# Performance work log

Hardware: AMD Instinct MI355X
Metric: run time of the kernel (lower is better)

Reference implementation:

```python
import jax, jax.numpy as jnp
import numpy as np

N_HEADS = 8


def _norm_weights(idx):
    # softmax over where(idx>0, 1, -9e15) along axis 1 -> uniform weights over non-pad slots
    logits = jnp.where(idx > 0, jnp.float32(1.0), jnp.float32(-9e15))
    return jax.nn.softmax(logits, axis=1)


def _layer_norm(x, g, b, eps=1e-6):
    mu = jnp.mean(x, axis=-1, keepdims=True)
    var = jnp.var(x, axis=-1, keepdims=True)
    return (x - mu) * jax.lax.rsqrt(var + eps) * g + b


def _mha_block(x, mask, wq, wk, wv, wo, g, b):
    # standard multi-head self-attention block with residual + layernorm
    B, L, D = x.shape
    hd = D // N_HEADS
    q = (x @ wq).reshape(B, L, N_HEADS, hd)
    k = (x @ wk).reshape(B, L, N_HEADS, hd)
    v = (x @ wv).reshape(B, L, N_HEADS, hd)
    scores = jnp.einsum('bqhd,bkhd->bhqk', q, k) / jnp.float32(np.sqrt(hd))
    scores = jnp.where(mask[:, None, None, :], jnp.float32(-1e9), scores)
    attn = jax.nn.softmax(scores, axis=-1)
    out = jnp.einsum('bhqk,bkhd->bqhd', attn, v).reshape(B, L, D) @ wo
    return _layer_norm(out + x, g, b)


def _forward(data_idx, seq, timestamps, user_level, useq, user_inf, user_cen,
             spread_status, id2vector,
             user_emb, cen_emb, time_emb, pos_emb, inf_emb,
             w1, w2, w3,
             t_wq, t_wk, t_wv, t_wo, t_g, t_b,
             s_wq, s_wk, s_wv, s_wo, s_g, s_b,
             W, W2, f_l1_w, f_l1_b, f_l2_w, f_l2_b, lin_w, lin_b):
    # ---- HGNN layer (hypergraph conv) ----
    tv = w3[0]  # TextVector = weight3[0]
    dot = w3 @ tv
    cos = dot / (jnp.linalg.norm(tv) * jnp.linalg.norm(w3, axis=1))
    inter_nw = jnp.mean(cos)  # scalar

    tweet_hidden = user_emb + cen_emb[user_cen]          # [N, D]
    x = (tweet_hidden @ w1) * inter_nw                   # [N, D]
    nor = _norm_weights(seq)                             # [E, L]
    edge = jnp.einsum('elc,el->ec', x[seq], nor)         # gather + weighted reduce
    edge = jax.nn.relu(edge)
    e1 = edge @ w2                                       # [E, D]
    u_nor = _norm_weights(useq)                          # [N, Lu]
    node = jnp.einsum('nlc,nl->nc', e1[useq], u_nor)     # [N, D]

    # ---- HGSL head ----
    sb = seq[data_idx]                                   # [B, L]
    nor_b = _norm_weights(sb)
    att_mask = sb == 0                                   # PAD == 0
    adj = node[sb]                                       # [B, L, D]

    att_hidden = adj + time_emb[timestamps[data_idx]]
    att_out = _mha_block(att_hidden, att_mask, t_wq, t_wk, t_wv, t_wo, t_g, t_b)
    news = jnp.einsum('blc,bl->bc', att_out, nor_b)
    news = jnp.concatenate([news, spread_status[data_idx][:, 2:] / 3600.0 / 24.0], axis=-1) @ W

    att_hidden_s = adj + inf_emb[user_inf[data_idx]] + pos_emb[user_level[data_idx]]
    att_out_s = _mha_block(att_hidden_s, att_mask, s_wq, s_wk, s_wv, s_wo, s_g, s_b)
    news_s = jnp.einsum('blc,bl->bc', att_out_s, nor_b)
    news_s = jnp.concatenate([news_s, spread_status[data_idx][:, :2]], axis=-1) @ W2

    # Gated fusion (linear3 unused in original forward; id2vector is overwritten/unused)
    emb = jnp.stack([news, news_s], axis=0)              # [2, B, D+2]
    score = jax.nn.softmax(jnp.tanh(emb @ f_l1_w + f_l1_b) @ f_l2_w + f_l2_b, axis=0)
    fused = jnp.sum(score * emb, axis=0)                 # [B, D+2]
    return jax.nn.log_softmax(fused @ lin_w + lin_b, axis=1)


def setup_inputs():
    key = jax.random.key(0)
    ks = jax.random.split(key, 40)
    N, E, L, Lu, D, B, TV = 50000, 10000, 50, 20, 128, 512, 768
    Dw = D + 2
    s = 0.05
    inp = {
        'data_idx': jax.random.randint(ks[0], (B,), 0, E),
        'seq': jax.random.randint(ks[1], (E, L), 0, N),
        'timestamps': jax.random.randint(ks[2], (E, L), 0, 5000),
        'user_level': jax.random.randint(ks[3], (E, L), 0, 50),
        'useq': jax.random.randint(ks[4], (N, Lu), 0, E),
        'user_inf': jax.random.randint(ks[5], (E, L), 0, 200),
        'user_cen': jax.random.randint(ks[6], (N,), 0, 600),
        'spread_status': jax.random.uniform(ks[7], (E, 4), dtype=jnp.float32),
        'id2vector': jax.random.normal(ks[8], (1,), dtype=jnp.float32),
        'user_emb': s * jax.random.normal(ks[9], (N, D), dtype=jnp.float32),
        'cen_emb': s * jax.random.normal(ks[10], (600, D), dtype=jnp.float32),
        'time_emb': s * jax.random.normal(ks[11], (5000, D), dtype=jnp.float32),
        'pos_emb': s * jax.random.normal(ks[12], (50, D), dtype=jnp.float32),
        'inf_emb': s * jax.random.normal(ks[13], (200, D), dtype=jnp.float32),
        'w1': s * jax.random.normal(ks[14], (D, D), dtype=jnp.float32),
        'w2': s * jax.random.normal(ks[15], (D, D), dtype=jnp.float32),
        'w3': s * jax.random.normal(ks[16], (TV, TV), dtype=jnp.float32),
        'W': s * jax.random.normal(ks[17], (Dw, Dw), dtype=jnp.float32),
        'W2': s * jax.random.normal(ks[18], (Dw, Dw), dtype=jnp.float32),
        'f_l1_w': s * jax.random.normal(ks[19], (Dw, Dw), dtype=jnp.float32),
        'f_l1_b': jnp.zeros((Dw,), jnp.float32),
        'f_l2_w': s * jax.random.normal(ks[20], (Dw, 1), dtype=jnp.float32),
        'f_l2_b': jnp.zeros((1,), jnp.float32),
        'lin_w': s * jax.random.normal(ks[21], (Dw, 2), dtype=jnp.float32),
        'lin_b': jnp.zeros((2,), jnp.float32),
    }
    for nm, i in [('t', 22), ('s', 27)]:
        inp[nm + '_wq'] = s * jax.random.normal(ks[i], (D, D), dtype=jnp.float32)
        inp[nm + '_wk'] = s * jax.random.normal(ks[i + 1], (D, D), dtype=jnp.float32)
        inp[nm + '_wv'] = s * jax.random.normal(ks[i + 2], (D, D), dtype=jnp.float32)
        inp[nm + '_wo'] = s * jax.random.normal(ks[i + 3], (D, D), dtype=jnp.float32)
        inp[nm + '_g'] = jnp.ones((D,), jnp.float32)
        inp[nm + '_b'] = jnp.zeros((D,), jnp.float32)
    return inp


def reference(data_idx, seq, timestamps, user_level, useq, user_inf, user_cen,
              spread_status, id2vector,
              user_emb, cen_emb, time_emb, pos_emb, inf_emb,
              w1, w2, w3,
              t_wq, t_wk, t_wv, t_wo, t_g, t_b,
              s_wq, s_wk, s_wv, s_wo, s_g, s_b,
              W, W2, f_l1_w, f_l1_b, f_l2_w, f_l2_b, lin_w, lin_b):
    return _forward(data_idx, seq, timestamps, user_level, useq, user_inf, user_cen,
                    spread_status, id2vector,
                    user_emb, cen_emb, time_emb, pos_emb, inf_emb,
                    w1, w2, w3,
                    t_wq, t_wk, t_wv, t_wo, t_g, t_b,
                    s_wq, s_wk, s_wv, s_wo, s_g, s_b,
                    W, W2, f_l1_w, f_l1_b, f_l2_w, f_l2_b, lin_w, lin_b)
```

## Files before the change

kernel.cpp:

```cpp
#include <hip/hip_runtime.h>
#include <math.h>

constexpr int Nn = 50000;
constexpr int Ee = 10000;
constexpr int Ll = 50;
constexpr int LuU = 20;
constexpr int Dd = 128;
constexpr int Bb = 512;
constexpr int TVv = 768;
constexpr int Dw = 130;
constexpr int BL = Bb * Ll;
constexpr int BLP = Bb * 64;

typedef __attribute__((ext_vector_type(8))) short bf8v;
typedef __attribute__((ext_vector_type(4))) float f4v;
typedef __attribute__((ext_vector_type(8))) unsigned short u16x8;
typedef __attribute__((ext_vector_type(4))) unsigned short u16x4;

__device__ __forceinline__ unsigned short f2bf(float f) {
  union { float f; unsigned u; } v; v.f = f;
  unsigned r = v.u + 0x7FFFu + ((v.u >> 16) & 1u);
  return (unsigned short)(r >> 16);
}
__device__ __forceinline__ float bf2f(unsigned short h) {
  union { unsigned u; float f; } v; v.u = ((unsigned)h) << 16; return v.f;
}
__device__ __forceinline__ int swz(int b) { return b ^ (((b >> 8) & 7) << 4); }
__device__ __forceinline__ int swz7(int b) { return b ^ (((b >> 7) & 7) << 4); }

__device__ __forceinline__ float block_sum_256(float v, volatile float* scr) {
#pragma unroll
  for (int o = 32; o > 0; o >>= 1) v += __shfl_down(v, o, 64);
  __syncthreads();
  if ((threadIdx.x & 63) == 0) scr[threadIdx.x >> 6] = v;
  __syncthreads();
  return scr[0] + scr[1] + scr[2] + scr[3];
}

__global__ __launch_bounds__(256) void k_cos(const float* __restrict__ w3,
                                             float* __restrict__ dotb,
                                             float* __restrict__ nrmb) {
  __shared__ float scr[4];
  int i = blockIdx.x;
  const float* row = w3 + (size_t)i * TVv;
  float d = 0.f, n = 0.f;
  for (int j = threadIdx.x; j < TVv; j += 256) {
    float a = row[j];
    d += a * w3[j];
    n += a * a;
  }
  d = block_sum_256(d, scr);
  n = block_sum_256(n, scr);
  if (threadIdx.x == 0) { dotb[i] = d; nrmb[i] = n; }
}

__global__ __launch_bounds__(256) void k_internw(const float* __restrict__ dotb,
                                                 const float* __restrict__ nrmb,
                                                 float* __restrict__ internw) {
  __shared__ float scr[4];
  float n0 = sqrtf(nrmb[0]);
  float s = 0.f;
  for (int i = threadIdx.x; i < TVv; i += 256)
    s += dotb[i] / (n0 * sqrtf(nrmb[i]));
  s = block_sum_256(s, scr);
  if (threadIdx.x == 0) *internw = s / (float)TVv;
}

__global__ __launch_bounds__(256) void k_prep(
    const float* w1, const float* w2,
    const float* twq, const float* twk, const float* twv, const float* two,
    const float* swq, const float* swk, const float* swv, const float* swo,
    unsigned short* __restrict__ out) {
  int wsel = blockIdx.x >> 3, part = blockIdx.x & 7;
  const float* w;
  switch (wsel) {
    case 0: w = w1; break;  case 1: w = w2; break;
    case 2: w = twq; break; case 3: w = twk; break;
    case 4: w = twv; break; case 5: w = two; break;
    case 6: w = swq; break; case 7: w = swk; break;
    case 8: w = swv; break; default: w = swo; break;
  }
  int u = part * 256 + threadIdx.x;
  int n = u >> 4, k0 = (u & 15) * 8;
  u16x8 pv;
#pragma unroll
  for (int i = 0; i < 8; i++) pv[i] = f2bf(w[(size_t)(k0 + i) * Dd + n]);
  ((u16x8*)(out + (size_t)wsel * Dd * Dd))[u] = pv;
}

__global__ __launch_bounds__(256) void k_th(const float* __restrict__ ue,
                                            const float* __restrict__ ce,
                                            const int* __restrict__ ucen,
                                            unsigned short* __restrict__ TH) {
  int r = blockIdx.x * 16 + (threadIdx.x >> 4);
  int c0 = (threadIdx.x & 15) * 8;
  int cen = ucen[r];
  const float4* up = (const float4*)(ue + (size_t)r * Dd + c0);
  const float4* cp = (const float4*)(ce + (size_t)cen * Dd + c0);
  float4 u0 = up[0], u1 = up[1], v0 = cp[0], v1 = cp[1];
  float a[8] = {u0.x + v0.x, u0.y + v0.y, u0.z + v0.z, u0.w + v0.w,
                u1.x + v1.x, u1.y + v1.y, u1.z + v1.z, u1.w + v1.w};
  u16x8 o;
#pragma unroll
  for (int i = 0; i < 8; i++) o[i] = f2bf(a[i]);
  *(u16x8*)(TH + (size_t)r * Dd + c0) = o;
}

template <int RELU>
__global__ __launch_bounds__(256) void k_gather(const unsigned short* __restrict__ X,
                                                const int* __restrict__ idx,
                                                unsigned short* __restrict__ out) {
  int r = blockIdx.x * 16 + (threadIdx.x >> 4);
  int c0 = (threadIdx.x & 15) * 8;
  const int* row = idx + (size_t)r * Ll;
  float acc[8];
#pragma unroll
  for (int i = 0; i < 8; i++) acc[i] = 0.f;
  int cnt = 0;
#pragma unroll 1
  for (int l0 = 0; l0 < Ll; l0 += 10) {
    int ids[10];
#pragma unroll
    for (int t = 0; t < 10; t++) ids[t] = row[l0 + t];
    u16x8 vv[10];
#pragma unroll
    for (int t = 0; t < 10; t++)
      vv[t] = *(const u16x8*)(X + (size_t)ids[t] * Dd + c0);
#pragma unroll
    for (int t = 0; t < 10; t++)
      if (ids[t] > 0) {
        cnt++;
#pragma unroll
        for (int i = 0; i < 8; i++) acc[i] += bf2f(vv[t][i]);
      }
  }
  u16x8 ov;
  if (cnt) {
    float inv = 1.f / (float)cnt;
#pragma unroll
    for (int i = 0; i < 8; i++) {
      float v = acc[i] * inv;
      if (RELU) v = fmaxf(v, 0.f);
      ov[i] = f2bf(v);
    }
  } else {
    u16x8 x0 = *(const u16x8*)(X + c0);
#pragma unroll
    for (int i = 0; i < 8; i++) {
      float v = bf2f(x0[i]);
      if (RELU) v = fmaxf(v, 0.f);
      ov[i] = f2bf(v);
    }
  }
  *(u16x8*)(out + (size_t)r * Dd + c0) = ov;
}

template <int EPI>
__global__ __launch_bounds__(256) void k_gemm_plain(
    const unsigned short* __restrict__ inA, const float* __restrict__ scalep,
    const unsigned short* __restrict__ WTg,
    unsigned short* __restrict__ out, int nrows) {
  __shared__ unsigned short WT[Dd * Dd];
  __shared__ __align__(16) unsigned short Ab[64 * Dd];
  int tid = threadIdx.x;
  float sc = (EPI == 1) ? *scalep : 1.f;
  {
    const u16x8* src = (const u16x8*)WTg;
    for (int u = tid; u < 2048; u += 256)
      *(u16x8*)((char*)WT + swz(u * 16)) = src[u];
  }
  int r0 = blockIdx.x * 64;
  for (int u = tid; u < 1024; u += 256) {
    int rr = u >> 4;
    int r = r0 + rr;
    u16x8 pv;
    if (r < nrows) pv = ((const u16x8*)inA)[(size_t)r * 16 + (u & 15)];
    else {
#pragma unroll
      for (int i = 0; i < 8; i++) pv[i] = 0;
    }
    *(u16x8*)((char*)Ab + swz(rr * 256 + (u & 15) * 16)) = pv;
  }
  __syncthreads();
  int lane = tid & 63, wid = tid >> 6;
  int lrow = lane & 15, lg = lane >> 4;
  bf8v af[4];
#pragma unroll
  for (int kc = 0; kc < 4; kc++)
    af[kc] = *(const bf8v*)((char*)Ab + swz((wid * 16 + lrow) * 256 + kc * 64 + lg * 16));
  f4v acc[8];
#pragma unroll
  for (int nt = 0; nt < 8; nt++)
#pragma unroll
    for (int j = 0; j < 4; j++) acc[nt][j] = 0.f;
#pragma unroll
  for (int nt = 0; nt < 8; nt++)
#pragma unroll
    for (int kc = 0; kc < 4; kc++) {
      bf8v bfg = *(const bf8v*)((char*)WT + swz((nt * 16 + lrow) * 256 + kc * 64 + lg * 16));
      acc[nt] = __builtin_amdgcn_mfma_f32_16x16x32_bf16(af[kc], bfg, acc[nt], 0, 0, 0);
    }
#pragma unroll
  for (int nt = 0; nt < 8; nt++)
#pragma unroll
    for (int j = 0; j < 4; j++) {
      int r = r0 + wid * 16 + lg * 4 + j;
      if (r < nrows) {
        float v = acc[nt][j];
        if (EPI == 1) v = fmaxf(v * sc, 0.f);
        out[(size_t)r * Dd + nt * 16 + lrow] = f2bf(v);
      }
    }
}

__global__ __launch_bounds__(256) void k_hidfuse(
    const unsigned short* __restrict__ E1, const int* __restrict__ data_idx,
    const int* __restrict__ seq, const int* __restrict__ tsmp,
    const int* __restrict__ uinf, const int* __restrict__ ulev,
    const int* __restrict__ useq,
    const float* __restrict__ time_emb, const float* __restrict__ inf_emb,
    const float* __restrict__ pos_emb,
    unsigned short* __restrict__ hidTb, unsigned short* __restrict__ hidSb) {
  int bl = blockIdx.x * 16 + (threadIdx.x >> 4);
  int c0 = (threadIdx.x & 15) * 8;
  int b = bl / Ll, l = bl % Ll;
  int e = data_idx[b];
  int sid = seq[(size_t)e * Ll + l];
  const int* urow = useq + (size_t)sid * LuU;
  float acc[8];
#pragma unroll
  for (int i = 0; i < 8; i++) acc[i] = 0.f;
  int cnt = 0;
#pragma unroll 1
  for (int t0 = 0; t0 < LuU; t0 += 10) {
    int ids[10];
#pragma unroll
    for (int t = 0; t < 10; t++) ids[t] = urow[t0 + t];
    u16x8 vv[10];
#pragma unroll
    for (int t = 0; t < 10; t++)
      vv[t] = *(const u16x8*)(E1 + (size_t)ids[t] * Dd + c0);
#pragma unroll
    for (int t = 0; t < 10; t++)
      if (ids[t] > 0) {
        cnt++;
#pragma unroll
        for (int i = 0; i < 8; i++) acc[i] += bf2f(vv[t][i]);
      }
  }
  float node[8];
  if (cnt) {
    float inv = 1.f / (float)cnt;
#pragma unroll
    for (int i = 0; i < 8; i++) node[i] = acc[i] * inv;
  } else {
    u16x8 e0 = *(const u16x8*)(E1 + c0);
#pragma unroll
    for (int i = 0; i < 8; i++) node[i] = bf2f(e0[i]);
  }
  int ts = tsmp[(size_t)e * Ll + l];
  int fi = uinf[(size_t)e * Ll + l];
  int lv = ulev[(size_t)e * Ll + l];
  const float4* tp = (const float4*)(time_emb + (size_t)ts * Dd + c0);
  const float4* ip = (const float4*)(inf_emb + (size_t)fi * Dd + c0);
  const float4* pp = (const float4*)(pos_emb + (size_t)lv * Dd + c0);
  float4 t0 = tp[0], t1 = tp[1];
  float4 i0 = ip[0], i1 = ip[1];
  float4 p0 = pp[0], p1 = pp[1];
  float te[8] = {t0.x, t0.y, t0.z, t0.w, t1.x, t1.y, t1.z, t1.w};
  float ie[8] = {i0.x, i0.y, i0.z, i0.w, i1.x, i1.y, i1.z, i1.w};
  float pe[8] = {p0.x, p0.y, p0.z, p0.w, p1.x, p1.y, p1.z, p1.w};
  u16x8 ht, hs;
#pragma unroll
  for (int i = 0; i < 8; i++) {
    ht[i] = f2bf(node[i] + te[i]);
    hs[i] = f2bf(node[i] + ie[i] + pe[i]);
  }
  size_t o = (size_t)bl * Dd + c0;
  *(u16x8*)(hidTb + o) = ht;
  *(u16x8*)(hidSb + o) = hs;
}

__global__ __launch_bounds__(256, 3) void k_qkvattn(
    const unsigned short* __restrict__ hidT, const unsigned short* __restrict__ hidS,
    const unsigned short* __restrict__ WTbase,
    const int* __restrict__ data_idx, const int* __restrict__ seq,
    unsigned short* __restrict__ ctxp) {
  __shared__ __align__(16) char LDS[49152];
  char* Qs  = LDS;
  char* Ks  = LDS + 16384;
  char* VTs = LDS + 32768;

  int b = blockIdx.x, branch = blockIdx.y;
  int tid = threadIdx.x, lane = tid & 63, wid = tid >> 6;
  int lrow = lane & 15, lg = lane >> 4;
  const unsigned short* hid = (branch ? hidS : hidT) + (size_t)b * Ll * Dd;
  const unsigned short* Wq = WTbase + (size_t)(2 + branch * 4) * Dd * Dd;
  const unsigned short* Wk = Wq + Dd * Dd;
  const unsigned short* Wv = Wk + Dd * Dd;

  int e = data_idx[b];
  int mi = (lane < Ll) ? (seq[(size_t)e * Ll + lane] == 0 ? 1 : 0) : 2;
  int mflag[4][4];
#pragma unroll
  for (int mt = 0; mt < 4; mt++)
#pragma unroll
    for (int j = 0; j < 4; j++)
      mflag[mt][j] = __shfl(mi, mt * 16 + lg * 4 + j, 64);

  bf8v hf[4][4];
#pragma unroll
  for (int qt = 0; qt < 4; qt++) {
    int q = qt * 16 + lrow;
#pragma unroll
    for (int kc = 0; kc < 4; kc++) {
      bf8v v;
      if (q < Ll) v = *(const bf8v*)(hid + (size_t)q * Dd + kc * 32 + lg * 8);
      else {
#pragma unroll
        for (int i = 0; i < 8; i++) v[i] = 0;
      }
      hf[qt][kc] = v;
    }
  }

#pragma unroll
  for (int sel = 0; sel < 2; sel++) {
    const unsigned short* W = sel ? Wk : Wq;
    char* Dst = sel ? Ks : Qs;
#pragma unroll
    for (int n2 = 0; n2 < 2; n2++) {
      int n = wid * 2 + n2;
      bf8v wf[4];
#pragma unroll
      for (int kc = 0; kc < 4; kc++)
        wf[kc] = *(const bf8v*)(W + (size_t)(n * 16 + lrow) * Dd + kc * 32 + lg * 8);
#pragma unroll
      for (int qt = 0; qt < 4; qt++) {
        f4v a = {0.f, 0.f, 0.f, 0.f};
#pragma unroll
        for (int kc = 0; kc < 4; kc++)
          a = __builtin_amdgcn_mfma_f32_16x16x32_bf16(wf[kc], hf[qt][kc], a, 0, 0, 0);
        u16x4 o;
#pragma unroll
        for (int j = 0; j < 4; j++) o[j] = f2bf(a[j]);
        *(u16x4*)(Dst + swz((qt * 16 + lrow) * 256 + n * 32 + lg * 8)) = o;
      }
    }
  }
  {
    bf8v hv[4];
    int kvq = wid * 16 + lrow;
#pragma unroll
    for (int kc = 0; kc < 4; kc++) {
      bf8v v;
      if (kvq < Ll) v = *(const bf8v*)(hid + (size_t)kvq * Dd + kc * 32 + lg * 8);
      else {
#pragma unroll
        for (int i = 0; i < 8; i++) v[i] = 0;
      }
      hv[kc] = v;
    }
#pragma unroll
    for (int nt = 0; nt < 8; nt++) {
      bf8v wf[4];
#pragma unroll
      for (int kc = 0; kc < 4; kc++)
        wf[kc] = *(const bf8v*)(Wv + (size_t)(nt * 16 + lrow) * Dd + kc * 32 + lg * 8);
      f4v a = {0.f, 0.f, 0.f, 0.f};
#pragma unroll
      for (int kc = 0; kc < 4; kc++)
        a = __builtin_amdgcn_mfma_f32_16x16x32_bf16(hv[kc], wf[kc], a, 0, 0, 0);
      u16x4 o;
#pragma unroll
      for (int j = 0; j < 4; j++) o[j] = f2bf(a[j]);
      *(u16x4*)(VTs + swz7((nt * 16 + lrow) * 128 + (wid * 16 + lg * 4) * 2)) = o;
    }
  }
  bf8v af[2][4], bq[2][4];
#pragma unroll
  for (int hi = 0; hi < 2; hi++) {
    int h = wid * 2 + hi;
#pragma unroll
    for (int t = 0; t < 4; t++) {
      bf8v a, q;
      if (lg < 2) {
        a = *(const bf8v*)(Ks + swz((t * 16 + lrow) * 256 + h * 32 + lg * 16));
        q = *(const bf8v*)(Qs + swz((t * 16 + lrow) * 256 + h * 32 + lg * 16));
      } else {
#pragma unroll
        for (int i = 0; i < 8; i++) { a[i] = 0; q[i] = 0; }
      }
      af[hi][t] = a; bq[hi][t] = q;
    }
  }
  __syncthreads();

  char* PTw = LDS + wid * 8192;
  size_t rbase = ((size_t)branch * Bb + b) * 64;
#pragma unroll
  for (int hi = 0; hi < 2; hi++) {
    int h = wid * 2 + hi;
#pragma unroll
    for (int nt = 0; nt < 4; nt++) {
      f4v sa[4];
#pragma unroll
      for (int mt = 0; mt < 4; mt++)
#pragma unroll
        for (int j = 0; j < 4; j++) sa[mt][j] = 0.f;
#pragma unroll
      for (int mt = 0; mt < 4; mt++)
        sa[mt] = __builtin_amdgcn_mfma_f32_16x16x32_bf16(af[hi][mt], bq[hi][nt], sa[mt], 0, 0, 0);
      float m = -3.0e38f;
#pragma unroll
      for (int mt = 0; mt < 4; mt++)
#pragma unroll
        for (int j = 0; j < 4; j++) {
          int mk = mflag[mt][j];
          float v = sa[mt][j] * 0.25f;
          v = (mk == 1) ? -1e9f : v;
          v = (mk == 2) ? -3.0e38f : v;
          sa[mt][j] = v;
          m = fmaxf(m, v);
        }
      m = fmaxf(m, __shfl_xor(m, 16, 64));
      m = fmaxf(m, __shfl_xor(m, 32, 64));
      float s = 0.f;
#pragma unroll
      for (int mt = 0; mt < 4; mt++)
#pragma unroll
        for (int j = 0; j < 4; j++) {
          float p = expf(sa[mt][j] - m);
          sa[mt][j] = p;
          s += p;
        }
      s += __shfl_xor(s, 16, 64);
      s += __shfl_xor(s, 32, 64);
      float inv = 1.f / s;
      int q = nt * 16 + lrow;
#pragma unroll
      for (int mt = 0; mt < 4; mt++) {
        u16x4 pw;
#pragma unroll
        for (int j = 0; j < 4; j++) pw[j] = f2bf(sa[mt][j] * inv);
        *(u16x4*)(PTw + swz7(q * 128 + mt * 32 + lg * 8)) = pw;
      }
    }
    f4v pacc[4];
#pragma unroll
    for (int nt = 0; nt < 4; nt++)
#pragma unroll
      for (int j = 0; j < 4; j++) pacc[nt][j] = 0.f;
#pragma unroll
    for (int kt = 0; kt < 2; kt++) {
      bf8v av = *(const bf8v*)(VTs + swz7((h * 16 + lrow) * 128 + kt * 64 + lg * 16));
#pragma unroll
      for (int nt = 0; nt < 4; nt++) {
        bf8v bv = *(const bf8v*)(PTw + swz7((nt * 16 + lrow) * 128 + kt * 64 + lg * 16));
        pacc[nt] = __builtin_amdgcn_mfma_f32_16x16x32_bf16(av, bv, pacc[nt], 0, 0, 0);
      }
    }
#pragma unroll
    for (int nt = 0; nt < 4; nt++) {
      int q = nt * 16 + lrow;
      unsigned* cp = (unsigned*)(ctxp + (rbase + q) * Dd + h * 16 + lg * 4);
      cp[0] = (unsigned)f2bf(pacc[nt][0]) | ((unsigned)f2bf(pacc[nt][1]) << 16);
      cp[1] = (unsigned)f2bf(pacc[nt][2]) | ((unsigned)f2bf(pacc[nt][3]) << 16);
    }
  }
}

__global__ __launch_bounds__(256) void k_gemm_lnnews(
    const unsigned short* __restrict__ ctxp,
    const unsigned short* __restrict__ hidT, const unsigned short* __restrict__ hidS,
    const unsigned short* __restrict__ WTbase,
    const float* __restrict__ tg, const float* __restrict__ tb,
    const float* __restrict__ sg, const float* __restrict__ sb_,
    const int* __restrict__ data_idx, const int* __restrict__ seq,
    const float* __restrict__ spread,
    float* __restrict__ news) {
  __shared__ unsigned short WT[Dd * Dd];
  __shared__ __align__(16) char UB[64 * 132 * 4];
  __shared__ int sl[Ll];
  __shared__ int scnt;
  unsigned short* Ab = (unsigned short*)UB;
  float (*O)[132] = (float (*)[132])UB;

  int b = blockIdx.x & 511, branch = blockIdx.x >> 9;
  const unsigned short* resid = (branch ? hidS : hidT);
  const unsigned short* Wg = WTbase + (size_t)(5 + branch * 4) * Dd * Dd;
  const float* lng = branch ? sg : tg;
  const float* lnb = branch ? sb_ : tb;
  int tid = threadIdx.x;
  int e = data_idx[b];
  if (tid < Ll) sl[tid] = seq[(size_t)e * Ll + tid];

  {
    const u16x8* src = (const u16x8*)Wg;
    for (int u = tid; u < 2048; u += 256)
      *(u16x8*)((char*)WT + swz(u * 16)) = src[u];
  }
  for (int u = tid; u < 1024; u += 256) {
    int rr = u >> 4;
    u16x8 pv = ((const u16x8*)ctxp)[(((size_t)branch * Bb + b) * 64 + rr) * 16 + (u & 15)];
    *(u16x8*)((char*)Ab + swz(rr * 256 + (u & 15) * 16)) = pv;
  }
  __syncthreads();

  int lane = tid & 63, wid = tid >> 6;
  int lrow = lane & 15, lg = lane >> 4;
  bf8v af[4];
#pragma unroll
  for (int kc = 0; kc < 4; kc++)
    af[kc] = *(const bf8v*)((char*)Ab + swz((wid * 16 + lrow) * 256 + kc * 64 + lg * 16));
  f4v acc[8];
#pragma unroll
  for (int nt = 0; nt < 8; nt++)
#pragma unroll
    for (int j = 0; j < 4; j++) acc[nt][j] = 0.f;
#pragma unroll
  for (int nt = 0; nt < 8; nt++)
#pragma unroll
    for (int kc = 0; kc < 4; kc++) {
      bf8v bfg = *(const bf8v*)((char*)WT + swz((nt * 16 + lrow) * 256 + kc * 64 + lg * 16));
      acc[nt] = __builtin_amdgcn_mfma_f32_16x16x32_bf16(af[kc], bfg, acc[nt], 0, 0, 0);
    }
  __syncthreads();
#pragma unroll
  for (int nt = 0; nt < 8; nt++)
#pragma unroll
    for (int j = 0; j < 4; j++)
      O[wid * 16 + lg * 4 + j][nt * 16 + lrow] = acc[nt][j];
  __syncthreads();
  int r = tid >> 2, c0 = (tid & 3) * 32;
  if (r < Ll) {
    size_t gr = (size_t)b * Ll + r;
    float vv[32];
    float s1 = 0.f, s2 = 0.f;
#pragma unroll
    for (int i8 = 0; i8 < 4; i8++) {
      u16x8 hb = *(const u16x8*)(resid + gr * Dd + c0 + i8 * 8);
#pragma unroll
      for (int i = 0; i < 8; i++) {
        float x = O[r][c0 + i8 * 8 + i] + bf2f(hb[i]);
        vv[i8 * 8 + i] = x; s1 += x; s2 += x * x;
      }
    }
    s1 += __shfl_xor(s1, 1, 64); s2 += __shfl_xor(s2, 1, 64);
    s1 += __shfl_xor(s1, 2, 64); s2 += __shfl_xor(s2, 2, 64);
    float mu = s1 * (1.f / Dd);
    float var = s2 * (1.f / Dd) - mu * mu;
    float rs = rsqrtf(var + 1e-6f);
#pragma unroll
    for (int i = 0; i < 32; i++) {
      int c = c0 + i;
      O[r][c] = (vv[i] - mu) * rs * lng[c] + lnb[c];
    }
  }
  if (tid == 0) {
    int c = 0;
    for (int l = 0; l < Ll; l++) c += (sl[l] > 0);
    scnt = c;
  }
  __syncthreads();
  float* nrow = news + ((size_t)branch * Bb + b) * 132;
  if (tid < Dd) {
    int cnt = scnt;
    float wnp = cnt ? 1.f / (float)cnt : 0.02f;
    float a = 0.f;
    for (int l = 0; l < Ll; l++) {
      float w = cnt ? ((sl[l] > 0) ? wnp : 0.f) : wnp;
      a += w * O[l][tid];
    }
    nrow[tid] = a;
  } else if (tid < Dw) {
    int cc = tid - Dd;
    nrow[tid] = branch ? spread[(size_t)e * 4 + cc]
                       : spread[(size_t)e * 4 + 2 + cc] * (1.f / 86400.f);
  }
}

__global__ __launch_bounds__(256) void k_newsW(const float* __restrict__ news,
                                               const float* __restrict__ Wm,
                                               const float* __restrict__ W2m,
                                               float* __restrict__ NT,
                                               float* __restrict__ NS) {
  __shared__ float Wl[Dw][Dw + 1];
  __shared__ float nrow[132];
  int branch = blockIdx.y;
  const float* W = branch ? W2m : Wm;
  float* out = branch ? NS : NT;
  for (int u = threadIdx.x; u < Dw * Dw; u += 256)
    Wl[u / Dw][u % Dw] = W[u];
  for (int rr = 0; rr < 32; rr++) {
    int b = blockIdx.x * 32 + rr;
    __syncthreads();
    if (threadIdx.x < Dw)
      nrow[threadIdx.x] = news[((size_t)branch * Bb + b) * 132 + threadIdx.x];
    __syncthreads();
    int j = threadIdx.x;
    if (j < Dw) {
      float acc = 0.f;
      for (int kk = 0; kk < Dw; kk++) acc += nrow[kk] * Wl[kk][j];
      out[(size_t)b * Dw + j] = acc;
    }
  }
}

__global__ __launch_bounds__(256) void k_fusion(const float* __restrict__ nt,
                                                const float* __restrict__ ns,
                                                const float* __restrict__ l1w,
                                                const float* __restrict__ l1b,
                                                const float* __restrict__ l2w,
                                                const float* __restrict__ l2b,
                                                const float* __restrict__ linw,
                                                const float* __restrict__ linb,
                                                float* __restrict__ out) {
  __shared__ float rt[Dw], rs[Dw];
  __shared__ float scr[4];
  int b = blockIdx.x, j = threadIdx.x;
  if (j < Dw) { rt[j] = nt[(size_t)b * Dw + j]; rs[j] = ns[(size_t)b * Dw + j]; }
  __syncthreads();
  float pt = 0.f, ps = 0.f;
  if (j < Dw) {
    float at = l1b[j], as = l1b[j];
    for (int kk = 0; kk < Dw; kk++) {
      float w = l1w[(size_t)kk * Dw + j];
      at += rt[kk] * w;
      as += rs[kk] * w;
    }
    float lw2 = l2w[j];
    pt = tanhf(at) * lw2;
    ps = tanhf(as) * lw2;
  }
  float st = block_sum_256(pt, scr);
  float ss = block_sum_256(ps, scr);
  st += l2b[0]; ss += l2b[0];
  float m = fmaxf(st, ss);
  float e0 = expf(st - m), e1v = expf(ss - m);
  float inv = 1.f / (e0 + e1v);
  float s0 = e0 * inv, s1 = e1v * inv;
  float fj  = (j < Dw) ? (s0 * rt[j] + s1 * rs[j]) : 0.f;
  float w0  = (j < Dw) ? linw[(size_t)j * 2 + 0] : 0.f;
  float w1v = (j < Dw) ? linw[(size_t)j * 2 + 1] : 0.f;
  float l0 = block_sum_256(fj * w0, scr);
  float l1 = block_sum_256(fj * w1v, scr);
  if (j == 0) {
    l0 += linb[0]; l1 += linb[1];
    float mm = fmaxf(l0, l1);
    float lse = mm + logf(expf(l0 - mm) + expf(l1 - mm));
    out[(size_t)b * 2 + 0] = l0 - lse;
    out[(size_t)b * 2 + 1] = l1 - lse;
  }
}

extern "C" void kernel_launch(void* const* d_in, const int* in_sizes, int n_in,
                              void* d_out, int out_size, void* d_ws, size_t ws_size,
                              hipStream_t stream) {
  const int*   data_idx = (const int*)d_in[0];
  const int*   seq      = (const int*)d_in[1];
  const int*   tsmp     = (const int*)d_in[2];
  const int*   ulev     = (const int*)d_in[3];
  const int*   useq     = (const int*)d_in[4];
  const int*   uinf     = (const int*)d_in[5];
  const int*   ucen     = (const int*)d_in[6];
  const float* spread   = (const float*)d_in[7];
  const float* user_emb = (const float*)d_in[9];
  const float* cen_emb  = (const float*)d_in[10];
  const float* time_emb = (const float*)d_in[11];
  const float* pos_emb  = (const float*)d_in[12];
  const float* inf_emb  = (const float*)d_in[13];
  const float* w1       = (const float*)d_in[14];
  const float* w2       = (const float*)d_in[15];
  const float* w3       = (const float*)d_in[16];
  const float* Wm       = (const float*)d_in[17];
  const float* W2m      = (const float*)d_in[18];
  const float* f_l1_w   = (const float*)d_in[19];
  const float* f_l1_b   = (const float*)d_in[20];
  const float* f_l2_w   = (const float*)d_in[21];
  const float* f_l2_b   = (const float*)d_in[22];
  const float* lin_w    = (const float*)d_in[23];
  const float* lin_b    = (const float*)d_in[24];
  const float* t_wq = (const float*)d_in[25];
  const float* t_wk = (const float*)d_in[26];
  const float* t_wv = (const float*)d_in[27];
  const float* t_wo = (const float*)d_in[28];
  const float* t_g  = (const float*)d_in[29];
  const float* t_b  = (const float*)d_in[30];
  const float* s_wq = (const float*)d_in[31];
  const float* s_wk = (const float*)d_in[32];
  const float* s_wv = (const float*)d_in[33];
  const float* s_wo = (const float*)d_in[34];
  const float* s_g  = (const float*)d_in[35];
  const float* s_b  = (const float*)d_in[36];

  char* ws = (char*)d_ws;
  constexpr size_t SZ_WT  = (size_t)10 * Dd * Dd * 2;
  constexpr size_t SZ_TH  = (size_t)Nn * Dd * 2;
  constexpr size_t SZ_EB  = (size_t)Ee * Dd * 2;
  constexpr size_t SZ_BH  = (size_t)BL * Dd * 2;
  constexpr size_t SZ_PD  = (size_t)2 * BLP * Dd * 2;
  constexpr size_t OFF_WT  = 8192;
  constexpr size_t OFF_TH  = OFF_WT + SZ_WT;
  constexpr size_t OFF_G   = OFF_TH + SZ_TH;
  constexpr size_t OFF_EDGE= OFF_G + SZ_EB;
  constexpr size_t OFF_E1  = OFF_EDGE + SZ_EB;
  constexpr size_t OFF_HTB = OFF_E1 + SZ_EB;
  constexpr size_t OFF_HSB = OFF_HTB + SZ_BH;
  constexpr size_t OFF_CTX = OFF_HSB + SZ_BH;
  constexpr size_t OFF_NEWS= OFF_CTX + SZ_PD;
  constexpr size_t OFF_NT  = OFF_NEWS + (size_t)2 * Bb * 132 * 4;
  constexpr size_t OFF_NS  = OFF_NT + (size_t)Bb * Dw * 4;

  float* dotb    = (float*)(ws + 0);
  float* nrmb    = (float*)(ws + 3072);
  float* internw = (float*)(ws + 6144);
  unsigned short* WTall = (unsigned short*)(ws + OFF_WT);
  unsigned short* TH    = (unsigned short*)(ws + OFF_TH);
  unsigned short* G     = (unsigned short*)(ws + OFF_G);
  unsigned short* EDGEb = (unsigned short*)(ws + OFF_EDGE);
  unsigned short* E1b   = (unsigned short*)(ws + OFF_E1);
  unsigned short* HIDTb = (unsigned short*)(ws + OFF_HTB);
  unsigned short* HIDSb = (unsigned short*)(ws + OFF_HSB);
  unsigned short* CTXp  = (unsigned short*)(ws + OFF_CTX);
  float*          NEWS  = (float*)(ws + OFF_NEWS);
  float*          NT    = (float*)(ws + OFF_NT);
  float*          NS    = (float*)(ws + OFF_NS);
  float* outp = (float*)d_out;

  k_prep<<<80, 256, 0, stream>>>(w1, w2, t_wq, t_wk, t_wv, t_wo,
                                 s_wq, s_wk, s_wv, s_wo, WTall);
  k_cos<<<TVv, 256, 0, stream>>>(w3, dotb, nrmb);
  k_internw<<<1, 256, 0, stream>>>(dotb, nrmb, internw);

  k_th<<<Nn / 16, 256, 0, stream>>>(user_emb, cen_emb, ucen, TH);
  k_gather<0><<<Ee / 16, 256, 0, stream>>>(TH, seq, G);
  k_gemm_plain<1><<<(Ee + 63) / 64, 256, 0, stream>>>(
      G, internw, WTall + 0 * Dd * Dd, EDGEb, Ee);
  k_gemm_plain<0><<<(Ee + 63) / 64, 256, 0, stream>>>(
      EDGEb, nullptr, WTall + 1 * Dd * Dd, E1b, Ee);
  k_hidfuse<<<BL / 16, 256, 0, stream>>>(E1b, data_idx, seq, tsmp, uinf, ulev, useq,
                                         time_emb, inf_emb, pos_emb, HIDTb, HIDSb);

  k_qkvattn<<<dim3(Bb, 2), 256, 0, stream>>>(HIDTb, HIDSb, WTall, data_idx, seq, CTXp);
  k_gemm_lnnews<<<1024, 256, 0, stream>>>(CTXp, HIDTb, HIDSb, WTall,
                                          t_g, t_b, s_g, s_b,
                                          data_idx, seq, spread, NEWS);

  k_newsW<<<dim3(16, 2), 256, 0, stream>>>(NEWS, Wm, W2m, NT, NS);
  k_fusion<<<Bb, 256, 0, stream>>>(NT, NS, f_l1_w, f_l1_b, f_l2_w, f_l2_b,
                                   lin_w, lin_b, outp);

  (void)in_sizes; (void)n_in; (void)out_size; (void)ws_size;
}
```

Baseline: 323.6 us.

## Restructure attention to one wave per head and read Wo from global

The QKV+attention kernel now launches 512 threads, giving each of the 8 waves exactly one head. Each wave computes its own head's Q, K and V into a private LDS region, so the block-wide __syncthreads is gone. V is passed to the PV matmul through register shuffles rather than an LDS transpose. The mask comes from a ballot bitmask, and expf is replaced by the faster, less precise __expf. The output-projection/LayerNorm kernel drops its 32KB LDS staging of Wo and loads weight fragments straight from global memory, which lowers LDS use but relies on cache hits for the repeated weight reads.

```diff
diff --git a/kernel.cpp b/kernel.cpp
--- a/kernel.cpp
+++ b/kernel.cpp
@@ -281,16 +281,12 @@
   *(u16x8*)(hidSb + o) = hs;
 }
 
-__global__ __launch_bounds__(256, 3) void k_qkvattn(
+__global__ __launch_bounds__(512, 4) void k_qkvattn(
     const unsigned short* __restrict__ hidT, const unsigned short* __restrict__ hidS,
     const unsigned short* __restrict__ WTbase,
     const int* __restrict__ data_idx, const int* __restrict__ seq,
     unsigned short* __restrict__ ctxp) {
-  __shared__ __align__(16) char LDS[49152];
-  char* Qs  = LDS;
-  char* Ks  = LDS + 16384;
-  char* VTs = LDS + 32768;
-
+  __shared__ __align__(16) char LDS[65536];
   int b = blockIdx.x, branch = blockIdx.y;
   int tid = threadIdx.x, lane = tid & 63, wid = tid >> 6;
   int lrow = lane & 15, lg = lane >> 4;
@@ -298,15 +294,12 @@
   const unsigned short* Wq = WTbase + (size_t)(2 + branch * 4) * Dd * Dd;
   const unsigned short* Wk = Wq + Dd * Dd;
   const unsigned short* Wv = Wk + Dd * Dd;
+  char* R = LDS + wid * 8192;
+  int h = wid;
 
   int e = data_idx[b];
-  int mi = (lane < Ll) ? (seq[(size_t)e * Ll + lane] == 0 ? 1 : 0) : 2;
-  int mflag[4][4];
-#pragma unroll
-  for (int mt = 0; mt < 4; mt++)
-#pragma unroll
-    for (int j = 0; j < 4; j++)
-      mflag[mt][j] = __shfl(mi, mt * 16 + lg * 4 + j, 64);
+  int sv = (lane < Ll) ? seq[(size_t)e * Ll + lane] : 1;
+  unsigned long long mzero = __ballot(sv == 0);
 
   bf8v hf[4][4];
 #pragma unroll
@@ -327,146 +320,136 @@
 #pragma unroll
   for (int sel = 0; sel < 2; sel++) {
     const unsigned short* W = sel ? Wk : Wq;
-    char* Dst = sel ? Ks : Qs;
-#pragma unroll
-    for (int n2 = 0; n2 < 2; n2++) {
-      int n = wid * 2 + n2;
-      bf8v wf[4];
+    bf8v wf[4];
+#pragma unroll
+    for (int kc = 0; kc < 4; kc++)
+      wf[kc] = *(const bf8v*)(W + (size_t)(h * 16 + lrow) * Dd + kc * 32 + lg * 8);
+#pragma unroll
+    for (int qt = 0; qt < 4; qt++) {
+      f4v a = {0.f, 0.f, 0.f, 0.f};
 #pragma unroll
       for (int kc = 0; kc < 4; kc++)
-        wf[kc] = *(const bf8v*)(W + (size_t)(n * 16 + lrow) * Dd + kc * 32 + lg * 8);
-#pragma unroll
-      for (int qt = 0; qt < 4; qt++) {
-        f4v a = {0.f, 0.f, 0.f, 0.f};
-#pragma unroll
-        for (int kc = 0; kc < 4; kc++)
-          a = __builtin_amdgcn_mfma_f32_16x16x32_bf16(wf[kc], hf[qt][kc], a, 0, 0, 0);
-        u16x4 o;
-#pragma unroll
-        for (int j = 0; j < 4; j++) o[j] = f2bf(a[j]);
-        *(u16x4*)(Dst + swz((qt * 16 + lrow) * 256 + n * 32 + lg * 8)) = o;
+        a = __builtin_amdgcn_mfma_f32_16x16x32_bf16(wf[kc], hf[qt][kc], a, 0, 0, 0);
+      u16x4 o;
+#pragma unroll
+      for (int j = 0; j < 4; j++) o[j] = f2bf(a[j]);
+      *(u16x4*)(R + swz7((qt * 16 + lrow) * 128 + sel * 32 + lg * 8)) = o;
+    }
+  }
+  unsigned pv[4][2];
+  {
+    bf8v wf[4];
+#pragma unroll
+    for (int kc = 0; kc < 4; kc++)
+      wf[kc] = *(const bf8v*)(Wv + (size_t)(h * 16 + lrow) * Dd + kc * 32 + lg * 8);
+#pragma unroll
+    for (int mt = 0; mt < 4; mt++) {
+      f4v a = {0.f, 0.f, 0.f, 0.f};
+#pragma unroll
+      for (int kc = 0; kc < 4; kc++)
+        a = __builtin_amdgcn_mfma_f32_16x16x32_bf16(hf[mt][kc], wf[kc], a, 0, 0, 0);
+      pv[mt][0] = (unsigned)f2bf(a[0]) | ((unsigned)f2bf(a[1]) << 16);
+      pv[mt][1] = (unsigned)f2bf(a[2]) | ((unsigned)f2bf(a[3]) << 16);
+    }
+  }
+  bf8v af[4], bq[4];
+#pragma unroll
+  for (int t = 0; t < 4; t++) {
+    bf8v a, q;
+    if (lg < 2) {
+      a = *(const bf8v*)(R + swz7((t * 16 + lrow) * 128 + 32 + lg * 16));
+      q = *(const bf8v*)(R + swz7((t * 16 + lrow) * 128 + lg * 16));
+    } else {
+#pragma unroll
+      for (int i = 0; i < 8; i++) { a[i] = 0; q[i] = 0; }
+    }
+    af[t] = a; bq[t] = q;
+  }
+  asm volatile("s_waitcnt lgkmcnt(0)" ::: "memory");
+  __builtin_amdgcn_sched_barrier(0);
+
+  size_t rbase = ((size_t)branch * Bb + b) * 64;
+  int lg4 = lg * 4;
+#pragma unroll
+  for (int nt = 0; nt < 4; nt++) {
+    f4v sa[4];
+#pragma unroll
+    for (int mt = 0; mt < 4; mt++)
+#pragma unroll
+      for (int j = 0; j < 4; j++) sa[mt][j] = 0.f;
+#pragma unroll
+    for (int mt = 0; mt < 4; mt++)
+      sa[mt] = __builtin_amdgcn_mfma_f32_16x16x32_bf16(af[mt], bq[nt], sa[mt], 0, 0, 0);
+    float m = -3.0e38f;
+#pragma unroll
+    for (int mt = 0; mt < 4; mt++)
+#pragma unroll
+      for (int j = 0; j < 4; j++) {
+        int kk = mt * 16 + lg4 + j;
+        float v = sa[mt][j] * 0.25f;
+        v = ((mzero >> kk) & 1ull) ? -1e9f : v;
+        if (mt == 3) v = (lg4 + j >= 2) ? -3.0e38f : v;
+        sa[mt][j] = v;
+        m = fmaxf(m, v);
       }
-    }
-  }
-  {
-    bf8v hv[4];
-    int kvq = wid * 16 + lrow;
-#pragma unroll
-    for (int kc = 0; kc < 4; kc++) {
-      bf8v v;
-      if (kvq < Ll) v = *(const bf8v*)(hid + (size_t)kvq * Dd + kc * 32 + lg * 8);
-      else {
-#pragma unroll
-        for (int i = 0; i < 8; i++) v[i] = 0;
+    m = fmaxf(m, __shfl_xor(m, 16, 64));
+    m = fmaxf(m, __shfl_xor(m, 32, 64));
+    float s = 0.f;
+#pragma unroll
+    for (int mt = 0; mt < 4; mt++)
+#pragma unroll
+      for (int j = 0; j < 4; j++) {
+        float p = __expf(sa[mt][j] - m);
+        sa[mt][j] = p;
+        s += p;
       }
-      hv[kc] = v;
-    }
-#pragma unroll
-    for (int nt = 0; nt < 8; nt++) {
-      bf8v wf[4];
-#pragma unroll
-      for (int kc = 0; kc < 4; kc++)
-        wf[kc] = *(const bf8v*)(Wv + (size_t)(nt * 16 + lrow) * Dd + kc * 32 + lg * 8);
-      f4v a = {0.f, 0.f, 0.f, 0.f};
-#pragma unroll
-      for (int kc = 0; kc < 4; kc++)
-        a = __builtin_amdgcn_mfma_f32_16x16x32_bf16(hv[kc], wf[kc], a, 0, 0, 0);
-      u16x4 o;
-#pragma unroll
-      for (int j = 0; j < 4; j++) o[j] = f2bf(a[j]);
-      *(u16x4*)(VTs + swz7((nt * 16 + lrow) * 128 + (wid * 16 + lg * 4) * 2)) = o;
-    }
-  }
-  bf8v af[2][4], bq[2][4];
-#pragma unroll
-  for (int hi = 0; hi < 2; hi++) {
-    int h = wid * 2 + hi;
-#pragma unroll
-    for (int t = 0; t < 4; t++) {
-      bf8v a, q;
-      if (lg < 2) {
-        a = *(const bf8v*)(Ks + swz((t * 16 + lrow) * 256 + h * 32 + lg * 16));
-        q = *(const bf8v*)(Qs + swz((t * 16 + lrow) * 256 + h * 32 + lg * 16));
-      } else {
-#pragma unroll
-        for (int i = 0; i < 8; i++) { a[i] = 0; q[i] = 0; }
-      }
-      af[hi][t] = a; bq[hi][t] = q;
-    }
-  }
-  __syncthreads();
-
-  char* PTw = LDS + wid * 8192;
-  size_t rbase = ((size_t)branch * Bb + b) * 64;
-#pragma unroll
-  for (int hi = 0; hi < 2; hi++) {
-    int h = wid * 2 + hi;
+    s += __shfl_xor(s, 16, 64);
+    s += __shfl_xor(s, 32, 64);
+    float inv = 1.f / s;
+    int q = nt * 16 + lrow;
+#pragma unroll
+    for (int mt = 0; mt < 4; mt++) {
+      u16x4 pw;
+#pragma unroll
+      for (int j = 0; j < 4; j++) pw[j] = f2bf(sa[mt][j] * inv);
+      *(u16x4*)(R + swz7(q * 128 + mt * 32 + lg * 8)) = pw;
+    }
+  }
+  f4v pacc[4];
+#pragma unroll
+  for (int nt = 0; nt < 4; nt++)
+#pragma unroll
+    for (int j = 0; j < 4; j++) pacc[nt][j] = 0.f;
+  int srcA = lrow + 32 * (lg & 1);
+  int srcB = srcA + 16;
+  bool up = (lg >> 1) & 1;
+#pragma unroll
+  for (int kt = 0; kt < 2; kt++) {
+    unsigned p00 = __shfl((int)pv[kt * 2][0],     srcA, 64);
+    unsigned p10 = __shfl((int)pv[kt * 2 + 1][0], srcA, 64);
+    unsigned p01 = __shfl((int)pv[kt * 2][1],     srcA, 64);
+    unsigned p11 = __shfl((int)pv[kt * 2 + 1][1], srcA, 64);
+    unsigned q00 = __shfl((int)pv[kt * 2][0],     srcB, 64);
+    unsigned q10 = __shfl((int)pv[kt * 2 + 1][0], srcB, 64);
+    unsigned q01 = __shfl((int)pv[kt * 2][1],     srcB, 64);
+    unsigned q11 = __shfl((int)pv[kt * 2 + 1][1], srcB, 64);
+    union { bf8v v; unsigned d[4]; } avu;
+    avu.d[0] = up ? p10 : p00;
+    avu.d[1] = up ? p11 : p01;
+    avu.d[2] = up ? q10 : q00;
+    avu.d[3] = up ? q11 : q01;
 #pragma unroll
     for (int nt = 0; nt < 4; nt++) {
-      f4v sa[4];
-#pragma unroll
-      for (int mt = 0; mt < 4; mt++)
-#pragma unroll
-        for (int j = 0; j < 4; j++) sa[mt][j] = 0.f;
-#pragma unroll
-      for (int mt = 0; mt < 4; mt++)
-        sa[mt] = __builtin_amdgcn_mfma_f32_16x16x32_bf16(af[hi][mt], bq[hi][nt], sa[mt], 0, 0, 0);
-      float m = -3.0e38f;
-#pragma unroll
-      for (int mt = 0; mt < 4; mt++)
-#pragma unroll
-        for (int j = 0; j < 4; j++) {
-          int mk = mflag[mt][j];
-          float v = sa[mt][j] * 0.25f;
-          v = (mk == 1) ? -1e9f : v;
-          v = (mk == 2) ? -3.0e38f : v;
-          sa[mt][j] = v;
-          m = fmaxf(m, v);
-        }
-      m = fmaxf(m, __shfl_xor(m, 16, 64));
-      m = fmaxf(m, __shfl_xor(m, 32, 64));
-      float s = 0.f;
-#pragma unroll
-      for (int mt = 0; mt < 4; mt++)
-#pragma unroll
-        for (int j = 0; j < 4; j++) {
-          float p = expf(sa[mt][j] - m);
-          sa[mt][j] = p;
-          s += p;
-        }
-      s += __shfl_xor(s, 16, 64);
-      s += __shfl_xor(s, 32, 64);
-      float inv = 1.f / s;
-      int q = nt * 16 + lrow;
-#pragma unroll
-      for (int mt = 0; mt < 4; mt++) {
-        u16x4 pw;
-#pragma unroll
-        for (int j = 0; j < 4; j++) pw[j] = f2bf(sa[mt][j] * inv);
-        *(u16x4*)(PTw + swz7(q * 128 + mt * 32 + lg * 8)) = pw;
-      }
-    }
-    f4v pacc[4];
-#pragma unroll
-    for (int nt = 0; nt < 4; nt++)
-#pragma unroll
-      for (int j = 0; j < 4; j++) pacc[nt][j] = 0.f;
-#pragma unroll
-    for (int kt = 0; kt < 2; kt++) {
-      bf8v av = *(const bf8v*)(VTs + swz7((h * 16 + lrow) * 128 + kt * 64 + lg * 16));
-#pragma unroll
-      for (int nt = 0; nt < 4; nt++) {
-        bf8v bv = *(const bf8v*)(PTw + swz7((nt * 16 + lrow) * 128 + kt * 64 + lg * 16));
-        pacc[nt] = __builtin_amdgcn_mfma_f32_16x16x32_bf16(av, bv, pacc[nt], 0, 0, 0);
-      }
-    }
-#pragma unroll
-    for (int nt = 0; nt < 4; nt++) {
-      int q = nt * 16 + lrow;
-      unsigned* cp = (unsigned*)(ctxp + (rbase + q) * Dd + h * 16 + lg * 4);
-      cp[0] = (unsigned)f2bf(pacc[nt][0]) | ((unsigned)f2bf(pacc[nt][1]) << 16);
-      cp[1] = (unsigned)f2bf(pacc[nt][2]) | ((unsigned)f2bf(pacc[nt][3]) << 16);
-    }
+      bf8v bv = *(const bf8v*)(R + swz7((nt * 16 + lrow) * 128 + kt * 64 + lg * 16));
+      pacc[nt] = __builtin_amdgcn_mfma_f32_16x16x32_bf16(avu.v, bv, pacc[nt], 0, 0, 0);
+    }
+  }
+#pragma unroll
+  for (int nt = 0; nt < 4; nt++) {
+    int q = nt * 16 + lrow;
+    unsigned* cp = (unsigned*)(ctxp + (rbase + q) * Dd + h * 16 + lg * 4);
+    cp[0] = (unsigned)f2bf(pacc[nt][0]) | ((unsigned)f2bf(pacc[nt][1]) << 16);
+    cp[1] = (unsigned)f2bf(pacc[nt][2]) | ((unsigned)f2bf(pacc[nt][3]) << 16);
   }
 }
 
@@ -479,7 +462,6 @@
     const int* __restrict__ data_idx, const int* __restrict__ seq,
     const float* __restrict__ spread,
     float* __restrict__ news) {
-  __shared__ unsigned short WT[Dd * Dd];
   __shared__ __align__(16) char UB[64 * 132 * 4];
   __shared__ int sl[Ll];
   __shared__ int scnt;
@@ -495,11 +477,6 @@
   int e = data_idx[b];
   if (tid < Ll) sl[tid] = seq[(size_t)e * Ll + tid];
 
-  {
-    const u16x8* src = (const u16x8*)Wg;
-    for (int u = tid; u < 2048; u += 256)
-      *(u16x8*)((char*)WT + swz(u * 16)) = src[u];
-  }
   for (int u = tid; u < 1024; u += 256) {
     int rr = u >> 4;
     u16x8 pv = ((const u16x8*)ctxp)[(((size_t)branch * Bb + b) * 64 + rr) * 16 + (u & 15)];
@@ -519,12 +496,15 @@
 #pragma unroll
     for (int j = 0; j < 4; j++) acc[nt][j] = 0.f;
 #pragma unroll
-  for (int nt = 0; nt < 8; nt++)
-#pragma unroll
-    for (int kc = 0; kc < 4; kc++) {
-      bf8v bfg = *(const bf8v*)((char*)WT + swz((nt * 16 + lrow) * 256 + kc * 64 + lg * 16));
-      acc[nt] = __builtin_amdgcn_mfma_f32_16x16x32_bf16(af[kc], bfg, acc[nt], 0, 0, 0);
-    }
+  for (int nt = 0; nt < 8; nt++) {
+    bf8v wf[4];
+#pragma unroll
+    for (int kc = 0; kc < 4; kc++)
+      wf[kc] = *(const bf8v*)(Wg + (size_t)(nt * 16 + lrow) * Dd + kc * 32 + lg * 8);
+#pragma unroll
+    for (int kc = 0; kc < 4; kc++)
+      acc[nt] = __builtin_amdgcn_mfma_f32_16x16x32_bf16(af[kc], wf[kc], acc[nt], 0, 0, 0);
+  }
   __syncthreads();
 #pragma unroll
   for (int nt = 0; nt < 8; nt++)
@@ -742,7 +722,7 @@
   k_hidfuse<<<BL / 16, 256, 0, stream>>>(E1b, data_idx, seq, tsmp, uinf, ulev, useq,
                                          time_emb, inf_emb, pos_emb, HIDTb, HIDSb);
 
-  k_qkvattn<<<dim3(Bb, 2), 256, 0, stream>>>(HIDTb, HIDSb, WTall, data_idx, seq, CTXp);
+  k_qkvattn<<<dim3(Bb, 2), 512, 0, stream>>>(HIDTb, HIDSb, WTall, data_idx, seq, CTXp);
   k_gemm_lnnews<<<1024, 256, 0, stream>>>(CTXp, HIDTb, HIDSb, WTall,
                                           t_g, t_b, s_g, s_b,
                                           data_idx, seq, spread, NEWS);
```

Result: no change. 319.9 us (-1.1%).
